# Optimization experiments

Measured on AMD Instinct MI355X. Metric: run time of the kernel, lower is better.

The kernel has to match this reference:

```python
import jax, jax.numpy as jnp
import numpy as np

ALPHA = 1.0

def setup_inputs() -> dict:
    key = jax.random.key(0)
    k1, k2, k3, k4 = jax.random.split(key, 4)
    B, N, D = 2048, 32768, 128
    return {
        "anchor": jax.random.normal(k1, (B, D), dtype=jnp.float32),
        "positive": jax.random.normal(k2, (B, D), dtype=jnp.float32),
        "negative": jax.random.normal(k3, (N, D), dtype=jnp.float32),
        "r_score": jax.random.normal(k4, (B, 1), dtype=jnp.float32),
    }

def reference(anchor, positive, negative, r_score):
    # pos_sim: [B,1] elementwise dot per row
    pos_sim = jnp.sum(anchor * positive, axis=1, keepdims=True)
    # neg_mul: [B,N] score matrix; row-wise stable logsumexp -> [B,1]
    neg_mul = jnp.matmul(anchor, negative.T)
    neg_sim = jax.scipy.special.logsumexp(neg_mul, axis=1, keepdims=True)
    loss = jax.nn.relu(neg_sim - pos_sim + r_score + ALPHA)
    return jnp.mean(loss)
```

## Files before the change

### kernel.cpp

```cpp
#include <hip/hip_runtime.h>
#include <hip/hip_bf16.h>


#define B_ROWS 2048
#define N_NEG  32768
#define DIM    128
#define LOG2E  1.4426950408889634f
#define LN2    0.6931471805599453f

typedef __bf16 bf16x8 __attribute__((ext_vector_type(8)));
typedef float  f32x4  __attribute__((ext_vector_type(4)));

static __device__ inline unsigned short f2bf(float f) {
    union { float f; unsigned u; } v; v.f = f;
    unsigned r = v.u + 0x7FFF + ((v.u >> 16) & 1);
    return (unsigned short)(r >> 16);
}

static __device__ inline void load_lds16(const void* g, void* s) {
    __builtin_amdgcn_global_load_lds(
        (const __attribute__((address_space(1))) void*)g,
        (__attribute__((address_space(3))) void*)s,
        16, 0, 0);
}

__global__ void prep_anchor(const float* __restrict__ anchor,
                            const float* __restrict__ positive,
                            unsigned short* __restrict__ a_bf,
                            float* __restrict__ pos_sim,
                            float* __restrict__ sumexp) {
    int t   = threadIdx.x;
    int row = blockIdx.x * 8 + (t >> 5);
    int c4  = (t & 31) * 4;
    const float4 a4 = *(const float4*)(anchor   + row * DIM + c4);
    const float4 p4 = *(const float4*)(positive + row * DIM + c4);
    float dot = a4.x * p4.x + a4.y * p4.y + a4.z * p4.z + a4.w * p4.w;
    ushort4 ab;
    ab.x = f2bf(a4.x * LOG2E); ab.y = f2bf(a4.y * LOG2E);
    ab.z = f2bf(a4.z * LOG2E); ab.w = f2bf(a4.w * LOG2E);
    *(ushort4*)(a_bf + row * DIM + c4) = ab;
    #pragma unroll
    for (int m = 1; m <= 16; m <<= 1) dot += __shfl_xor(dot, m, 64);
    if ((t & 31) == 0) { pos_sim[row] = dot; sumexp[row] = 0.0f; }
}

__global__ void conv_neg(const float* __restrict__ neg,
                         unsigned short* __restrict__ n_bf) {
    int i = blockIdx.x * 256 + threadIdx.x;
    #pragma unroll
    for (int k = 0; k < 4; k++) {
        int idx = i + k * (1024 * 256);
        float4 v = *(const float4*)(neg + (size_t)idx * 4);
        ushort4 o;
        o.x = f2bf(v.x); o.y = f2bf(v.y); o.z = f2bf(v.z); o.w = f2bf(v.w);
        *(ushort4*)(n_bf + (size_t)idx * 4) = o;
    }
}

#define CHUNK 1024
#define TSTEPS (CHUNK / 128)

__global__ __launch_bounds__(256, 2) void fused_gemm_lse(
        const unsigned short* __restrict__ A,
        const unsigned short* __restrict__ Nb,
        float* __restrict__ sumexp) {
    __shared__ unsigned short lds[2][128 * 128];

    const int bid     = blockIdx.x;
    const int rowTile = bid & 15;
    const int chunk   = bid >> 4;
    const int wave = threadIdx.x >> 6, lane = threadIdx.x & 63;
    const int wr = wave >> 1, wc = wave & 1;
    const int q = lane >> 4, c = lane & 15;

    const unsigned short* Ag = A + rowTile * (128 * DIM);
    const unsigned short* Bg = Nb + (size_t)(chunk * CHUNK) * DIM;
    #pragma unroll
    for (int i = 0; i < 8; i++) {
        int off = wave * 4096 + i * 512;
        load_lds16(Ag + off + lane * 8, &lds[0][off]);
        load_lds16(Bg + off + lane * 8, &lds[1][off]);
    }
    asm volatile("s_waitcnt vmcnt(0)" ::: "memory");
    __syncthreads();

    bf16x8 af[4][4];
    #pragma unroll
    for (int i = 0; i < 4; i++)
        #pragma unroll
        for (int k = 0; k < 4; k++)
            af[i][k] = *(const bf16x8*)&lds[0][(wr * 64 + i * 16 + c) * DIM + k * 32 + q * 8];
    __syncthreads();

    const f32x4 zero4 = {0.f, 0.f, 0.f, 0.f};
    f32x4 sumacc[4] = {zero4, zero4, zero4, zero4};

    for (int t = 0; t < TSTEPS; t++) {
        const int cur = 1 - (t & 1);
        const int nxt = t & 1;
        if (t + 1 < TSTEPS) {
            const unsigned short* Bn = Bg + (size_t)(t + 1) * 128 * DIM;
            #pragma unroll
            for (int i = 0; i < 8; i++) {
                int off = wave * 4096 + i * 512;
                load_lds16(Bn + off + lane * 8, &lds[nxt][off]);
            }
        }
        #pragma unroll
        for (int j = 0; j < 4; j++) {
            bf16x8 bf[4];
            #pragma unroll
            for (int k = 0; k < 4; k++)
                bf[k] = *(const bf16x8*)&lds[cur][(wc * 64 + j * 16 + c) * DIM + k * 32 + q * 8];
            #pragma unroll
            for (int i = 0; i < 4; i++) {
                f32x4 acc = __builtin_amdgcn_mfma_f32_16x16x32_bf16(af[i][0], bf[0], zero4, 0, 0, 0);
                acc = __builtin_amdgcn_mfma_f32_16x16x32_bf16(af[i][1], bf[1], acc, 0, 0, 0);
                acc = __builtin_amdgcn_mfma_f32_16x16x32_bf16(af[i][2], bf[2], acc, 0, 0, 0);
                acc = __builtin_amdgcn_mfma_f32_16x16x32_bf16(af[i][3], bf[3], acc, 0, 0, 0);
                sumacc[i][0] += exp2f(acc[0]);
                sumacc[i][1] += exp2f(acc[1]);
                sumacc[i][2] += exp2f(acc[2]);
                sumacc[i][3] += exp2f(acc[3]);
            }
        }
        asm volatile("s_waitcnt vmcnt(0)" ::: "memory");
        __syncthreads();
    }

    #pragma unroll
    for (int i = 0; i < 4; i++) {
        #pragma unroll
        for (int r = 0; r < 4; r++) {
            float v = sumacc[i][r];
            v += __shfl_xor(v, 1, 64);
            v += __shfl_xor(v, 2, 64);
            v += __shfl_xor(v, 4, 64);
            v += __shfl_xor(v, 8, 64);
            if ((lane & 15) == 0) {
                int row = rowTile * 128 + wr * 64 + i * 16 + q * 4 + r;
                atomicAdd(&sumexp[row], v);
            }
        }
    }
}

__global__ void finalize(const float* __restrict__ sumexp,
                         const float* __restrict__ pos_sim,
                         const float* __restrict__ r_score,
                         float* __restrict__ out) {
    __shared__ float red[4];
    int t = threadIdx.x;
    float acc = 0.0f;
    #pragma unroll
    for (int i = 0; i < 8; i++) {
        int row = t + i * 256;
        float lse  = __log2f(sumexp[row]) * LN2;
        float loss = lse - pos_sim[row] + r_score[row] + 1.0f;
        acc += fmaxf(loss, 0.0f);
    }
    #pragma unroll
    for (int m = 1; m <= 32; m <<= 1) acc += __shfl_xor(acc, m, 64);
    if ((t & 63) == 0) red[t >> 6] = acc;
    __syncthreads();
    if (t == 0) out[0] = (red[0] + red[1] + red[2] + red[3]) * (1.0f / (float)B_ROWS);
}

extern "C" void kernel_launch(void* const* d_in, const int* in_sizes, int n_in,
                              void* d_out, int out_size, void* d_ws, size_t ws_size,
                              hipStream_t stream) {
    const float* anchor   = (const float*)d_in[0];
    const float* positive = (const float*)d_in[1];
    const float* negative = (const float*)d_in[2];
    const float* r_score  = (const float*)d_in[3];
    float* out = (float*)d_out;

    char* ws = (char*)d_ws;
    float* sumexp           = (float*)ws;
    float* pos_sim          = (float*)(ws + 8192);
    unsigned short* a_bf    = (unsigned short*)(ws + 16384);
    unsigned short* n_bf    = (unsigned short*)(ws + 16384 + 524288);

    prep_anchor<<<256, 256, 0, stream>>>(anchor, positive, a_bf, pos_sim, sumexp);
    conv_neg<<<1024, 256, 0, stream>>>(negative, n_bf);
    fused_gemm_lse<<<512, 256, 0, stream>>>(a_bf, n_bf, sumexp);
    finalize<<<1, 256, 0, stream>>>(sumexp, pos_sim, r_score, out);
}
```

Before: 108.5 us.

## Swizzle LDS tiles, merge prep kernels, use raw exp2, skip final barrier

The global-to-LDS loads now use an XOR swizzle on the 16-byte chunk index per row, and the fragment reads apply the matching swizzle. This targets LDS bank conflicts from 256-byte row strides in the MFMA operand reads. The anchor prep and negative conversion kernels become one launch, saving a kernel launch and its gap. exp2f is replaced by the hardware exp2 builtin, which drops range-handling code and may lose accuracy for extreme inputs. The trailing wait and barrier are skipped on the last tile.

Result: faster. 95.44 us (-12.0%).

```diff
diff --git a/kernel.cpp b/kernel.cpp
--- a/kernel.cpp
+++ b/kernel.cpp
@@ -24,36 +24,37 @@
         16, 0, 0);
 }
 
-__global__ void prep_anchor(const float* __restrict__ anchor,
-                            const float* __restrict__ positive,
-                            unsigned short* __restrict__ a_bf,
-                            float* __restrict__ pos_sim,
-                            float* __restrict__ sumexp) {
-    int t   = threadIdx.x;
-    int row = blockIdx.x * 8 + (t >> 5);
-    int c4  = (t & 31) * 4;
-    const float4 a4 = *(const float4*)(anchor   + row * DIM + c4);
-    const float4 p4 = *(const float4*)(positive + row * DIM + c4);
-    float dot = a4.x * p4.x + a4.y * p4.y + a4.z * p4.z + a4.w * p4.w;
-    ushort4 ab;
-    ab.x = f2bf(a4.x * LOG2E); ab.y = f2bf(a4.y * LOG2E);
-    ab.z = f2bf(a4.z * LOG2E); ab.w = f2bf(a4.w * LOG2E);
-    *(ushort4*)(a_bf + row * DIM + c4) = ab;
-    #pragma unroll
-    for (int m = 1; m <= 16; m <<= 1) dot += __shfl_xor(dot, m, 64);
-    if ((t & 31) == 0) { pos_sim[row] = dot; sumexp[row] = 0.0f; }
-}
-
-__global__ void conv_neg(const float* __restrict__ neg,
-                         unsigned short* __restrict__ n_bf) {
-    int i = blockIdx.x * 256 + threadIdx.x;
-    #pragma unroll
-    for (int k = 0; k < 4; k++) {
-        int idx = i + k * (1024 * 256);
-        float4 v = *(const float4*)(neg + (size_t)idx * 4);
-        ushort4 o;
-        o.x = f2bf(v.x); o.y = f2bf(v.y); o.z = f2bf(v.z); o.w = f2bf(v.w);
-        *(ushort4*)(n_bf + (size_t)idx * 4) = o;
+__global__ void prep(const float* __restrict__ anchor,
+                     const float* __restrict__ positive,
+                     const float* __restrict__ neg,
+                     unsigned short* __restrict__ a_bf,
+                     unsigned short* __restrict__ n_bf,
+                     float* __restrict__ pos_sim,
+                     float* __restrict__ sumexp) {
+    int t = threadIdx.x;
+    if (blockIdx.x < 256) {
+        int row = blockIdx.x * 8 + (t >> 5);
+        int c4  = (t & 31) * 4;
+        const float4 a4 = *(const float4*)(anchor   + row * DIM + c4);
+        const float4 p4 = *(const float4*)(positive + row * DIM + c4);
+        float dot = a4.x * p4.x + a4.y * p4.y + a4.z * p4.z + a4.w * p4.w;
+        ushort4 ab;
+        ab.x = f2bf(a4.x * LOG2E); ab.y = f2bf(a4.y * LOG2E);
+        ab.z = f2bf(a4.z * LOG2E); ab.w = f2bf(a4.w * LOG2E);
+        *(ushort4*)(a_bf + row * DIM + c4) = ab;
+        #pragma unroll
+        for (int m = 1; m <= 16; m <<= 1) dot += __shfl_xor(dot, m, 64);
+        if ((t & 31) == 0) { pos_sim[row] = dot; sumexp[row] = 0.0f; }
+    } else {
+        int i = (blockIdx.x - 256) * 256 + t;
+        #pragma unroll
+        for (int k = 0; k < 4; k++) {
+            int idx = i + k * (1024 * 256);
+            float4 v = *(const float4*)(neg + (size_t)idx * 4);
+            ushort4 o;
+            o.x = f2bf(v.x); o.y = f2bf(v.y); o.z = f2bf(v.z); o.w = f2bf(v.w);
+            *(ushort4*)(n_bf + (size_t)idx * 4) = o;
+        }
     }
 }
 
@@ -72,24 +73,35 @@
     const int wave = threadIdx.x >> 6, lane = threadIdx.x & 63;
     const int wr = wave >> 1, wc = wave & 1;
     const int q = lane >> 4, c = lane & 15;
+    const int lrow = lane >> 4;
+    const int lchk = lane & 15;
 
     const unsigned short* Ag = A + rowTile * (128 * DIM);
     const unsigned short* Bg = Nb + (size_t)(chunk * CHUNK) * DIM;
+
     #pragma unroll
     for (int i = 0; i < 8; i++) {
         int off = wave * 4096 + i * 512;
-        load_lds16(Ag + off + lane * 8, &lds[0][off]);
-        load_lds16(Bg + off + lane * 8, &lds[1][off]);
+        int r   = (off >> 7) + lrow;
+        int gofs = r * DIM + ((lchk ^ (r & 7)) << 3);
+        load_lds16(Ag + gofs, &lds[0][off]);
+        load_lds16(Bg + gofs, &lds[1][off]);
     }
     asm volatile("s_waitcnt vmcnt(0)" ::: "memory");
     __syncthreads();
 
+    int swz[4];
+    #pragma unroll
+    for (int k = 0; k < 4; k++) swz[k] = (((k * 4 + q) ^ (c & 7)) << 3);
+
     bf16x8 af[4][4];
     #pragma unroll
-    for (int i = 0; i < 4; i++)
+    for (int i = 0; i < 4; i++) {
+        int row = wr * 64 + i * 16 + c;
         #pragma unroll
         for (int k = 0; k < 4; k++)
-            af[i][k] = *(const bf16x8*)&lds[0][(wr * 64 + i * 16 + c) * DIM + k * 32 + q * 8];
+            af[i][k] = *(const bf16x8*)&lds[0][row * DIM + swz[k]];
+    }
     __syncthreads();
 
     const f32x4 zero4 = {0.f, 0.f, 0.f, 0.f};
@@ -103,29 +115,34 @@
             #pragma unroll
             for (int i = 0; i < 8; i++) {
                 int off = wave * 4096 + i * 512;
-                load_lds16(Bn + off + lane * 8, &lds[nxt][off]);
+                int r   = (off >> 7) + lrow;
+                int gofs = r * DIM + ((lchk ^ (r & 7)) << 3);
+                load_lds16(Bn + gofs, &lds[nxt][off]);
             }
         }
         #pragma unroll
         for (int j = 0; j < 4; j++) {
+            int brow = wc * 64 + j * 16 + c;
             bf16x8 bf[4];
             #pragma unroll
             for (int k = 0; k < 4; k++)
-                bf[k] = *(const bf16x8*)&lds[cur][(wc * 64 + j * 16 + c) * DIM + k * 32 + q * 8];
+                bf[k] = *(const bf16x8*)&lds[cur][brow * DIM + swz[k]];
             #pragma unroll
             for (int i = 0; i < 4; i++) {
                 f32x4 acc = __builtin_amdgcn_mfma_f32_16x16x32_bf16(af[i][0], bf[0], zero4, 0, 0, 0);
                 acc = __builtin_amdgcn_mfma_f32_16x16x32_bf16(af[i][1], bf[1], acc, 0, 0, 0);
                 acc = __builtin_amdgcn_mfma_f32_16x16x32_bf16(af[i][2], bf[2], acc, 0, 0, 0);
                 acc = __builtin_amdgcn_mfma_f32_16x16x32_bf16(af[i][3], bf[3], acc, 0, 0, 0);
-                sumacc[i][0] += exp2f(acc[0]);
-                sumacc[i][1] += exp2f(acc[1]);
-                sumacc[i][2] += exp2f(acc[2]);
-                sumacc[i][3] += exp2f(acc[3]);
+                sumacc[i][0] += __builtin_amdgcn_exp2f(acc[0]);
+                sumacc[i][1] += __builtin_amdgcn_exp2f(acc[1]);
+                sumacc[i][2] += __builtin_amdgcn_exp2f(acc[2]);
+                sumacc[i][3] += __builtin_amdgcn_exp2f(acc[3]);
             }
         }
-        asm volatile("s_waitcnt vmcnt(0)" ::: "memory");
-        __syncthreads();
+        if (t + 1 < TSTEPS) {
+            asm volatile("s_waitcnt vmcnt(0)" ::: "memory");
+            __syncthreads();
+        }
     }
 
     #pragma unroll
@@ -181,8 +198,7 @@
     unsigned short* a_bf    = (unsigned short*)(ws + 16384);
     unsigned short* n_bf    = (unsigned short*)(ws + 16384 + 524288);
 
-    prep_anchor<<<256, 256, 0, stream>>>(anchor, positive, a_bf, pos_sim, sumexp);
-    conv_neg<<<1024, 256, 0, stream>>>(negative, n_bf);
+    prep<<<1280, 256, 0, stream>>>(anchor, positive, negative, a_bf, n_bf, pos_sim, sumexp);
     fused_gemm_lse<<<512, 256, 0, stream>>>(a_bf, n_bf, sumexp);
     finalize<<<1, 256, 0, stream>>>(sumexp, pos_sim, r_score, out);
 }
```
